# Optimization experiments

Measured on AMD Instinct MI355X. Metric: run time of the kernel, lower is better.

The kernel has to match this reference:

```python
import jax, jax.numpy as jnp
import numpy as np

B, N = 1, 320  # embed_dim == seq_len == N is forced by the module's bmm shapes


def setup_inputs() -> dict:
    key = jax.random.key(0)
    k1, k2, k3, k4 = jax.random.split(key, 4)
    s = jax.random.normal(k1, (B, N, N), dtype=jnp.float32)
    futrue = jax.random.normal(k2, (B, N, N, N), dtype=jnp.float32)
    # nn.Linear(embed_dim, embed_dim) params
    lim = 1.0 / np.sqrt(N)
    W = jax.random.uniform(k3, (N, N), minval=-lim, maxval=lim, dtype=jnp.float32)
    b = jax.random.uniform(k4, (N,), minval=-lim, maxval=lim, dtype=jnp.float32)
    return {"s": s, "futrue": futrue, "W": W, "b": b}


def reference(s, futrue, W, b):
    # futrue = self.fc(futrue): Linear on last dim  [B,T,T,E]
    futP = jnp.einsum('bitj,ej->bite', futrue, W) + b
    # fc = s.transpose(1,2) @ futrue : [B,1,E,T] @ [B,T,T,E] -> [B,T,E,E]
    scores = jnp.einsum('bte,bitj->biej', s, futP)
    fc = jax.nn.softmax(scores, axis=-1)          # softmax over last dim
    # vectorized loop: t_i = fc[:, i].sum(1).unsqueeze(-2).bmm(s)
    w = fc.sum(axis=2)                            # [B, T, T] (sum over e)
    out = jnp.einsum('bij,bjk->bik', w, s)        # concat of all t_i -> [B, T, E]
    return out
```

## Files before the change

kernel.cpp:

```cpp
#include <hip/hip_runtime.h>
#include <hip/hip_bf16.h>
#include <math.h>

#define N 320
#define NN (N * N)
#define SST 324
#define ZCNT (NN + N)

typedef float f32x16 __attribute__((ext_vector_type(16)));
typedef short s16x8  __attribute__((ext_vector_type(8)));

#define MFMA32(a, b, c) __builtin_amdgcn_mfma_f32_32x32x16_bf16((a), (b), (c), 0, 0, 0)

union U4V { uint4 q; s16x8 v; };
union UAV { unsigned u[4]; s16x8 v; };

__device__ inline void split2(float x0, float x1, unsigned& hi, unsigned& lo) {
    unsigned u0 = __float_as_uint(x0), u1 = __float_as_uint(x1);
    hi = (u0 >> 16) | (u1 & 0xFFFF0000u);
    float d0 = x0 - __uint_as_float(u0 & 0xFFFF0000u);
    float d1 = x1 - __uint_as_float(u1 & 0xFFFF0000u);
    lo = (__float_as_uint(d0) >> 16) | (__float_as_uint(d1) & 0xFFFF0000u);
}

__global__ __launch_bounds__(256) void zero_w_kernel(float* __restrict__ w) {
    int idx = blockIdx.x * 256 + threadIdx.x;
    if (idx * 4 < ZCNT) ((float4*)w)[idx] = make_float4(0.f, 0.f, 0.f, 0.f);
}

__global__ __launch_bounds__(64) void colsum_kernel(const float* __restrict__ s,
                                                    float* __restrict__ colsum) {
    int e = blockIdx.x * 64 + threadIdx.x;
    int t0 = blockIdx.y * 40;
    float a[8];
#pragma unroll
    for (int u = 0; u < 8; ++u) a[u] = 0.f;
    for (int t = 0; t < 40; t += 8) {
#pragma unroll
        for (int u = 0; u < 8; ++u) a[u] += s[(size_t)(t0 + t + u) * N + e];
    }
    float sum = ((a[0] + a[1]) + (a[2] + a[3])) + ((a[4] + a[5]) + (a[6] + a[7]));
    atomicAdd(&colsum[e], sum);
}

__global__ __launch_bounds__(64) void pack_s_kernel(const float* __restrict__ s,
                                                    uint4* __restrict__ spH,
                                                    uint4* __restrict__ spL) {
    int blk = blockIdx.x;
    int l = threadIdx.x;
    int et = blk / 20, ts = blk % 20;
    int e = et * 32 + (l & 31);
    int t0 = ts * 16 + (l >> 5) * 8;
    unsigned hi[4], lo[4];
#pragma unroll
    for (int d = 0; d < 4; ++d)
        split2(s[(size_t)(t0 + 2 * d) * N + e], s[(size_t)(t0 + 2 * d + 1) * N + e],
               hi[d], lo[d]);
    spH[blk * 64 + l] = make_uint4(hi[0], hi[1], hi[2], hi[3]);
    spL[blk * 64 + l] = make_uint4(lo[0], lo[1], lo[2], lo[3]);
}

__global__ __launch_bounds__(64) void pack_w_kernel(const float* __restrict__ W,
                                                    uint4* __restrict__ wpH,
                                                    uint4* __restrict__ wpL) {
    int blk = blockIdx.x;
    int l = threadIdx.x;
    int jt = blk / 20, ks = blk % 20;
    int j = jt * 32 + (l & 31);
    int k0 = ks * 16 + (l >> 5) * 8;
    const float* wr = W + (size_t)j * N + k0;
    unsigned hi[4], lo[4];
#pragma unroll
    for (int d = 0; d < 4; ++d) split2(wr[2 * d], wr[2 * d + 1], hi[d], lo[d]);
    wpH[blk * 64 + l] = make_uint4(hi[0], hi[1], hi[2], hi[3]);
    wpL[blk * 64 + l] = make_uint4(lo[0], lo[1], lo[2], lo[3]);
}

__global__ __launch_bounds__(640, 5) void fused_kernel(
    const float* __restrict__ fut,
    const uint4* __restrict__ spH, const uint4* __restrict__ spL,
    const uint4* __restrict__ wpH, const uint4* __restrict__ wpL,
    const float* __restrict__ bvec, const float* __restrict__ colsum,
    float* __restrict__ w)
{
    const int bid = blockIdx.x;
    const int i   = (bid / 80) * 8 + (bid & 7);
    const int et  = (bid >> 3) % 10;
    const int tid = threadIdx.x;
    const int wid = tid >> 6;
    const int lane = tid & 63;
    const int l31 = lane & 31;
    const int hf  = lane >> 5;

    __shared__ union {
        unsigned short G[2][40 * 32 * 8];
        float S[32 * SST];
    } sm;
    __shared__ float csh[32];
    __shared__ float Mfin[32];
    __shared__ float Ifin[32];

    if (tid < 32) csh[tid] = colsum[et * 32 + tid];

    f32x16 acc;
#pragma unroll
    for (int r = 0; r < 16; ++r) acc[r] = 0.f;

    const float* fbase = fut + (size_t)i * NN + (size_t)(hf * 8) * N + wid * 32 + l31;
    const uint4* aH = spH + (size_t)(et * 20) * 64 + lane;
    const uint4* aL = spL + (size_t)(et * 20) * 64 + lane;

    for (int ts = 0; ts < 20; ++ts) {
        const float* fp = fbase + (size_t)(ts * 16) * N;
        float f[8];
#pragma unroll
        for (int j = 0; j < 8; ++j) f[j] = fp[j * N];
        U4V ah; ah.q = aH[ts * 64];
        U4V al; al.q = aL[ts * 64];
        UAV bh, bl;
#pragma unroll
        for (int d = 0; d < 4; ++d) split2(f[2 * d], f[2 * d + 1], bh.u[d], bl.u[d]);
        acc = MFMA32(ah.v, bh.v, acc);
        acc = MFMA32(al.v, bh.v, acc);
        acc = MFMA32(ah.v, bl.v, acc);
    }

    {
        const int c  = wid * 4 + (l31 >> 3);
        const int jj = l31 & 7;
        const int sw = c & 7;
        unsigned short* GH = sm.G[0];
        unsigned short* GL = sm.G[1];
#pragma unroll
        for (int r = 0; r < 16; ++r) {
            int e = (r & 3) + ((r >> 2) << 3) + (hf << 2);
            float x = acc[r];
            unsigned u = __float_as_uint(x);
            float d = x - __uint_as_float(u & 0xFFFF0000u);
            int off = (c * 32 + (e ^ sw)) * 8 + jj;
            GH[off] = (unsigned short)(u >> 16);
            GL[off] = (unsigned short)(__float_as_uint(d) >> 16);
        }
    }
    __syncthreads();

    f32x16 acc2;
#pragma unroll
    for (int r = 0; r < 16; ++r) acc2[r] = 0.f;

    const uint4* bH = wpH + (size_t)(wid * 20) * 64 + lane;
    const uint4* bL = wpL + (size_t)(wid * 20) * 64 + lane;
    const unsigned short* GH = sm.G[0];
    const unsigned short* GL = sm.G[1];

#pragma unroll 4
    for (int ks = 0; ks < 20; ++ks) {
        int c0 = ks * 2 + hf;
        int aoff = (c0 * 32 + (l31 ^ (c0 & 7))) * 8;
        s16x8 gah = *(const s16x8*)&GH[aoff];
        s16x8 gal = *(const s16x8*)&GL[aoff];
        U4V wh; wh.q = bH[ks * 64];
        U4V wl; wl.q = bL[ks * 64];
        acc2 = MFMA32(gah, wh.v, acc2);
        acc2 = MFMA32(gal, wh.v, acc2);
        acc2 = MFMA32(gah, wl.v, acc2);
    }

    const int jcol = wid * 32 + l31;
    float bj = bvec[jcol];
    float v[16];
#pragma unroll
    for (int r = 0; r < 16; ++r) {
        int e = (r & 3) + ((r >> 2) << 3) + (hf << 2);
        v[r] = acc2[r] + csh[e] * bj;
    }

    __syncthreads();

#pragma unroll
    for (int r = 0; r < 16; ++r) {
        int e = (r & 3) + ((r >> 2) << 3) + (hf << 2);
        sm.S[e * SST + jcol] = v[r];
    }
    __syncthreads();

    const int hw = tid >> 5;
    const int li = tid & 31;
    if (hw < 16) {
#pragma unroll
        for (int rr = 0; rr < 2; ++rr) {
            int row = 2 * hw + rr;
            float x[10];
            float m = -3.4e38f;
#pragma unroll
            for (int q = 0; q < 10; ++q) {
                x[q] = sm.S[row * SST + li + 32 * q];
                m = fmaxf(m, x[q]);
            }
#pragma unroll
            for (int off = 16; off; off >>= 1) m = fmaxf(m, __shfl_xor(m, off, 64));
            float ssum = 0.f;
#pragma unroll
            for (int q = 0; q < 10; ++q) ssum += __expf(x[q] - m);
#pragma unroll
            for (int off = 16; off; off >>= 1) ssum += __shfl_xor(ssum, off, 64);
            if (li == 0) { Mfin[row] = m; Ifin[row] = 1.0f / ssum; }
        }
    }
    __syncthreads();

    float wcol = 0.f;
#pragma unroll
    for (int r = 0; r < 16; ++r) {
        int e = (r & 3) + ((r >> 2) << 3) + (hf << 2);
        wcol += __expf(v[r] - Mfin[e]) * Ifin[e];
    }
    wcol += __shfl_xor(wcol, 32, 64);
    if (hf == 0) atomicAdd(&w[(size_t)i * N + jcol], wcol);
}

__global__ __launch_bounds__(320) void out_gemm_kernel(
    const float* __restrict__ w, const float* __restrict__ s,
    float* __restrict__ out)
{
    const int i = blockIdx.x;
    const int k = threadIdx.x;
    const float* wr = w + (size_t)i * N;
    float a0 = 0.f, a1 = 0.f, a2 = 0.f, a3 = 0.f;
    for (int j = 0; j < N; j += 4) {
        a0 += wr[j + 0] * s[(size_t)(j + 0) * N + k];
        a1 += wr[j + 1] * s[(size_t)(j + 1) * N + k];
        a2 += wr[j + 2] * s[(size_t)(j + 2) * N + k];
        a3 += wr[j + 3] * s[(size_t)(j + 3) * N + k];
    }
    out[(size_t)i * N + k] = (a0 + a1) + (a2 + a3);
}

extern "C" void kernel_launch(void* const* d_in, const int* in_sizes, int n_in,
                              void* d_out, int out_size, void* d_ws, size_t ws_size,
                              hipStream_t stream)
{
    const float* s    = (const float*)d_in[0];
    const float* fut  = (const float*)d_in[1];
    const float* W    = (const float*)d_in[2];
    const float* bvec = (const float*)d_in[3];
    float* out = (float*)d_out;

    char* base = (char*)d_ws;
    float* wbuf   = (float*)base;
    float* colsum = (float*)(base + 409600);
    uint4* spH = (uint4*)(base + 410880);
    uint4* spL = (uint4*)(base + 615680);
    uint4* wpH = (uint4*)(base + 820480);
    uint4* wpL = (uint4*)(base + 1025280);

    zero_w_kernel<<<dim3((ZCNT / 4 + 255) / 256), dim3(256), 0, stream>>>(wbuf);
    colsum_kernel<<<dim3(5, 8), dim3(64), 0, stream>>>(s, colsum);
    pack_s_kernel<<<dim3(200), dim3(64), 0, stream>>>(s, spH, spL);
    pack_w_kernel<<<dim3(200), dim3(64), 0, stream>>>(W, wpH, wpL);

    fused_kernel<<<dim3(3200), dim3(640), 0, stream>>>(
        fut, spH, spL, wpH, wpL, bvec, colsum, wbuf);

    out_gemm_kernel<<<dim3(N), dim3(320), 0, stream>>>(wbuf, s, out);
}
```

Measured before the change: 386.7 us.

## Process two e-tiles per block to halve futrue reads and fuse prep kernels

The main kernel now computes two 32-wide e slabs per block from one pass over the futrue tile, so each futrue element is loaded and split into bf16 hi/lo half as often and the grid shrinks from 3200 to 1600 blocks. The four small setup kernels are merged into one prep kernel, which also zeroes the output buffer, cutting launch overhead. The output GEMM is split four ways over j and accumulates with atomics for more parallelism. In exchange, the main kernel holds two MFMA accumulators, which raises register pressure, and it runs the softmax stage twice with extra block barriers.

Result: slower. 414.7 us (+7.2%).

```diff
diff --git a/kernel.cpp b/kernel.cpp
--- a/kernel.cpp
+++ b/kernel.cpp
@@ -5,7 +5,6 @@
 #define N 320
 #define NN (N * N)
 #define SST 324
-#define ZCNT (NN + N)
 
 typedef float f32x16 __attribute__((ext_vector_type(16)));
 typedef short s16x8  __attribute__((ext_vector_type(8)));
@@ -23,60 +22,60 @@
     lo = (__float_as_uint(d0) >> 16) | (__float_as_uint(d1) & 0xFFFF0000u);
 }
 
-__global__ __launch_bounds__(256) void zero_w_kernel(float* __restrict__ w) {
-    int idx = blockIdx.x * 256 + threadIdx.x;
-    if (idx * 4 < ZCNT) ((float4*)w)[idx] = make_float4(0.f, 0.f, 0.f, 0.f);
-}
-
-__global__ __launch_bounds__(64) void colsum_kernel(const float* __restrict__ s,
-                                                    float* __restrict__ colsum) {
-    int e = blockIdx.x * 64 + threadIdx.x;
-    int t0 = blockIdx.y * 40;
-    float a[8];
-#pragma unroll
-    for (int u = 0; u < 8; ++u) a[u] = 0.f;
-    for (int t = 0; t < 40; t += 8) {
-#pragma unroll
-        for (int u = 0; u < 8; ++u) a[u] += s[(size_t)(t0 + t + u) * N + e];
+__global__ __launch_bounds__(256) void prep_kernel(
+    const float* __restrict__ s, const float* __restrict__ W,
+    float* __restrict__ wbuf, float* __restrict__ out, float* __restrict__ colsum,
+    uint4* __restrict__ spH, uint4* __restrict__ spL,
+    uint4* __restrict__ wpH, uint4* __restrict__ wpL)
+{
+    const int bid = blockIdx.x;
+    const int tid = threadIdx.x;
+    if (bid < 100) {
+        ((float4*)wbuf)[bid * 256 + tid] = make_float4(0.f, 0.f, 0.f, 0.f);
+    } else if (bid < 200) {
+        ((float4*)out)[(bid - 100) * 256 + tid] = make_float4(0.f, 0.f, 0.f, 0.f);
+    } else if (bid < 202) {
+        int e = (bid - 200) * 256 + tid;
+        if (e < N) {
+            const float* sp = s + e;
+            float a[8];
+#pragma unroll
+            for (int u = 0; u < 8; ++u) a[u] = 0.f;
+            for (int t = 0; t < N; t += 8) {
+#pragma unroll
+                for (int u = 0; u < 8; ++u) a[u] += sp[(size_t)(t + u) * N];
+            }
+            colsum[e] = ((a[0] + a[1]) + (a[2] + a[3])) + ((a[4] + a[5]) + (a[6] + a[7]));
+        }
+    } else if (bid < 252) {
+        int sub = (bid - 202) * 4 + (tid >> 6);
+        int l = tid & 63;
+        int et = sub / 20, ts = sub % 20;
+        int e = et * 32 + (l & 31);
+        int t0 = ts * 16 + (l >> 5) * 8;
+        unsigned hi[4], lo[4];
+#pragma unroll
+        for (int d = 0; d < 4; ++d)
+            split2(s[(size_t)(t0 + 2 * d) * N + e], s[(size_t)(t0 + 2 * d + 1) * N + e],
+                   hi[d], lo[d]);
+        spH[sub * 64 + l] = make_uint4(hi[0], hi[1], hi[2], hi[3]);
+        spL[sub * 64 + l] = make_uint4(lo[0], lo[1], lo[2], lo[3]);
+    } else {
+        int sub = (bid - 252) * 4 + (tid >> 6);
+        int l = tid & 63;
+        int jt = sub / 20, ks = sub % 20;
+        int j = jt * 32 + (l & 31);
+        int k0 = ks * 16 + (l >> 5) * 8;
+        const float* wr = W + (size_t)j * N + k0;
+        unsigned hi[4], lo[4];
+#pragma unroll
+        for (int d = 0; d < 4; ++d) split2(wr[2 * d], wr[2 * d + 1], hi[d], lo[d]);
+        wpH[sub * 64 + l] = make_uint4(hi[0], hi[1], hi[2], hi[3]);
+        wpL[sub * 64 + l] = make_uint4(lo[0], lo[1], lo[2], lo[3]);
     }
-    float sum = ((a[0] + a[1]) + (a[2] + a[3])) + ((a[4] + a[5]) + (a[6] + a[7]));
-    atomicAdd(&colsum[e], sum);
-}
-
-__global__ __launch_bounds__(64) void pack_s_kernel(const float* __restrict__ s,
-                                                    uint4* __restrict__ spH,
-                                                    uint4* __restrict__ spL) {
-    int blk = blockIdx.x;
-    int l = threadIdx.x;
-    int et = blk / 20, ts = blk % 20;
-    int e = et * 32 + (l & 31);
-    int t0 = ts * 16 + (l >> 5) * 8;
-    unsigned hi[4], lo[4];
-#pragma unroll
-    for (int d = 0; d < 4; ++d)
-        split2(s[(size_t)(t0 + 2 * d) * N + e], s[(size_t)(t0 + 2 * d + 1) * N + e],
-               hi[d], lo[d]);
-    spH[blk * 64 + l] = make_uint4(hi[0], hi[1], hi[2], hi[3]);
-    spL[blk * 64 + l] = make_uint4(lo[0], lo[1], lo[2], lo[3]);
-}
-
-__global__ __launch_bounds__(64) void pack_w_kernel(const float* __restrict__ W,
-                                                    uint4* __restrict__ wpH,
-                                                    uint4* __restrict__ wpL) {
-    int blk = blockIdx.x;
-    int l = threadIdx.x;
-    int jt = blk / 20, ks = blk % 20;
-    int j = jt * 32 + (l & 31);
-    int k0 = ks * 16 + (l >> 5) * 8;
-    const float* wr = W + (size_t)j * N + k0;
-    unsigned hi[4], lo[4];
-#pragma unroll
-    for (int d = 0; d < 4; ++d) split2(wr[2 * d], wr[2 * d + 1], hi[d], lo[d]);
-    wpH[blk * 64 + l] = make_uint4(hi[0], hi[1], hi[2], hi[3]);
-    wpL[blk * 64 + l] = make_uint4(lo[0], lo[1], lo[2], lo[3]);
-}
-
-__global__ __launch_bounds__(640, 5) void fused_kernel(
+}
+
+__global__ __launch_bounds__(640, 5) void fused5_kernel(
     const float* __restrict__ fut,
     const uint4* __restrict__ spH, const uint4* __restrict__ spL,
     const uint4* __restrict__ wpH, const uint4* __restrict__ wpL,
@@ -84,8 +83,10 @@
     float* __restrict__ w)
 {
     const int bid = blockIdx.x;
-    const int i   = (bid / 80) * 8 + (bid & 7);
-    const int et  = (bid >> 3) % 10;
+    const int x  = bid & 7;
+    const int g  = bid >> 3;
+    const int iw = g / 5, eq = g % 5;
+    const int i  = iw * 8 + x;
     const int tid = threadIdx.x;
     const int wid = tid >> 6;
     const int lane = tid & 63;
@@ -96,125 +97,137 @@
         unsigned short G[2][40 * 32 * 8];
         float S[32 * SST];
     } sm;
-    __shared__ float csh[32];
+    __shared__ float csh[64];
     __shared__ float Mfin[32];
     __shared__ float Ifin[32];
 
-    if (tid < 32) csh[tid] = colsum[et * 32 + tid];
-
-    f32x16 acc;
-#pragma unroll
-    for (int r = 0; r < 16; ++r) acc[r] = 0.f;
+    if (tid < 64) csh[tid] = colsum[eq * 64 + tid];
+
+    f32x16 acc0, acc1;
+#pragma unroll
+    for (int r = 0; r < 16; ++r) { acc0[r] = 0.f; acc1[r] = 0.f; }
 
     const float* fbase = fut + (size_t)i * NN + (size_t)(hf * 8) * N + wid * 32 + l31;
-    const uint4* aH = spH + (size_t)(et * 20) * 64 + lane;
-    const uint4* aL = spL + (size_t)(et * 20) * 64 + lane;
-
+    const uint4* aH0 = spH + (size_t)((eq * 2 + 0) * 20) * 64 + lane;
+    const uint4* aL0 = spL + (size_t)((eq * 2 + 0) * 20) * 64 + lane;
+    const uint4* aH1 = spH + (size_t)((eq * 2 + 1) * 20) * 64 + lane;
+    const uint4* aL1 = spL + (size_t)((eq * 2 + 1) * 20) * 64 + lane;
+
+#pragma unroll 2
     for (int ts = 0; ts < 20; ++ts) {
         const float* fp = fbase + (size_t)(ts * 16) * N;
         float f[8];
 #pragma unroll
-        for (int j = 0; j < 8; ++j) f[j] = fp[j * N];
-        U4V ah; ah.q = aH[ts * 64];
-        U4V al; al.q = aL[ts * 64];
+        for (int m = 0; m < 8; ++m) f[m] = fp[(size_t)m * N];
         UAV bh, bl;
 #pragma unroll
         for (int d = 0; d < 4; ++d) split2(f[2 * d], f[2 * d + 1], bh.u[d], bl.u[d]);
-        acc = MFMA32(ah.v, bh.v, acc);
-        acc = MFMA32(al.v, bh.v, acc);
-        acc = MFMA32(ah.v, bl.v, acc);
+        U4V a0h, a0l, a1h, a1l;
+        a0h.q = aH0[ts * 64]; a0l.q = aL0[ts * 64];
+        a1h.q = aH1[ts * 64]; a1l.q = aL1[ts * 64];
+        acc0 = MFMA32(a0h.v, bh.v, acc0);
+        acc1 = MFMA32(a1h.v, bh.v, acc1);
+        acc0 = MFMA32(a0l.v, bh.v, acc0);
+        acc1 = MFMA32(a1l.v, bh.v, acc1);
+        acc0 = MFMA32(a0h.v, bl.v, acc0);
+        acc1 = MFMA32(a1h.v, bl.v, acc1);
     }
 
-    {
-        const int c  = wid * 4 + (l31 >> 3);
-        const int jj = l31 & 7;
-        const int sw = c & 7;
-        unsigned short* GH = sm.G[0];
-        unsigned short* GL = sm.G[1];
+    const uint4* bHp = wpH + (size_t)(wid * 20) * 64 + lane;
+    const uint4* bLp = wpL + (size_t)(wid * 20) * 64 + lane;
+    const int jcol = wid * 32 + l31;
+    const float bj = bvec[jcol];
+    const int hw = tid >> 5;
+    const int li = tid & 31;
+    float wcol = 0.f;
+
+    auto doSlab = [&](const f32x16& acc, const int slab) {
+        {
+            const int c  = wid * 4 + (l31 >> 3);
+            const int jj = l31 & 7;
+            const int sw = c & 7;
+            unsigned short* GH = sm.G[0];
+            unsigned short* GL = sm.G[1];
+#pragma unroll
+            for (int r = 0; r < 16; ++r) {
+                int e = (r & 3) + ((r >> 2) << 3) + (hf << 2);
+                float xv = acc[r];
+                unsigned u = __float_as_uint(xv);
+                float d = xv - __uint_as_float(u & 0xFFFF0000u);
+                int off = (c * 32 + (e ^ sw)) * 8 + jj;
+                GH[off] = (unsigned short)(u >> 16);
+                GL[off] = (unsigned short)(__float_as_uint(d) >> 16);
+            }
+        }
+        __syncthreads();
+
+        f32x16 p;
+#pragma unroll
+        for (int r = 0; r < 16; ++r) p[r] = 0.f;
+        const unsigned short* GH = sm.G[0];
+        const unsigned short* GL = sm.G[1];
+#pragma unroll 4
+        for (int ks = 0; ks < 20; ++ks) {
+            int c = ks * 2 + hf;
+            int off = (c * 32 + (l31 ^ (c & 7))) * 8;
+            s16x8 gh = *(const s16x8*)&GH[off];
+            s16x8 gl = *(const s16x8*)&GL[off];
+            U4V wh, wl;
+            wh.q = bHp[ks * 64];
+            wl.q = bLp[ks * 64];
+            p = MFMA32(gh, wh.v, p);
+            p = MFMA32(gl, wh.v, p);
+            p = MFMA32(gh, wl.v, p);
+        }
+
+        float v[16];
 #pragma unroll
         for (int r = 0; r < 16; ++r) {
             int e = (r & 3) + ((r >> 2) << 3) + (hf << 2);
-            float x = acc[r];
-            unsigned u = __float_as_uint(x);
-            float d = x - __uint_as_float(u & 0xFFFF0000u);
-            int off = (c * 32 + (e ^ sw)) * 8 + jj;
-            GH[off] = (unsigned short)(u >> 16);
-            GL[off] = (unsigned short)(__float_as_uint(d) >> 16);
-        }
-    }
-    __syncthreads();
-
-    f32x16 acc2;
-#pragma unroll
-    for (int r = 0; r < 16; ++r) acc2[r] = 0.f;
-
-    const uint4* bH = wpH + (size_t)(wid * 20) * 64 + lane;
-    const uint4* bL = wpL + (size_t)(wid * 20) * 64 + lane;
-    const unsigned short* GH = sm.G[0];
-    const unsigned short* GL = sm.G[1];
-
-#pragma unroll 4
-    for (int ks = 0; ks < 20; ++ks) {
-        int c0 = ks * 2 + hf;
-        int aoff = (c0 * 32 + (l31 ^ (c0 & 7))) * 8;
-        s16x8 gah = *(const s16x8*)&GH[aoff];
-        s16x8 gal = *(const s16x8*)&GL[aoff];
-        U4V wh; wh.q = bH[ks * 64];
-        U4V wl; wl.q = bL[ks * 64];
-        acc2 = MFMA32(gah, wh.v, acc2);
-        acc2 = MFMA32(gal, wh.v, acc2);
-        acc2 = MFMA32(gah, wl.v, acc2);
-    }
-
-    const int jcol = wid * 32 + l31;
-    float bj = bvec[jcol];
-    float v[16];
-#pragma unroll
-    for (int r = 0; r < 16; ++r) {
-        int e = (r & 3) + ((r >> 2) << 3) + (hf << 2);
-        v[r] = acc2[r] + csh[e] * bj;
-    }
-
-    __syncthreads();
-
-#pragma unroll
-    for (int r = 0; r < 16; ++r) {
-        int e = (r & 3) + ((r >> 2) << 3) + (hf << 2);
-        sm.S[e * SST + jcol] = v[r];
-    }
-    __syncthreads();
-
-    const int hw = tid >> 5;
-    const int li = tid & 31;
-    if (hw < 16) {
-#pragma unroll
-        for (int rr = 0; rr < 2; ++rr) {
-            int row = 2 * hw + rr;
-            float x[10];
-            float m = -3.4e38f;
-#pragma unroll
-            for (int q = 0; q < 10; ++q) {
-                x[q] = sm.S[row * SST + li + 32 * q];
-                m = fmaxf(m, x[q]);
+            v[r] = p[r] + csh[slab * 32 + e] * bj;
+        }
+        __syncthreads();
+
+#pragma unroll
+        for (int r = 0; r < 16; ++r) {
+            int e = (r & 3) + ((r >> 2) << 3) + (hf << 2);
+            sm.S[e * SST + jcol] = v[r];
+        }
+        __syncthreads();
+
+        if (hw < 16) {
+#pragma unroll
+            for (int rr = 0; rr < 2; ++rr) {
+                int row = 2 * hw + rr;
+                float xr[10];
+                float m = -3.4e38f;
+#pragma unroll
+                for (int q = 0; q < 10; ++q) {
+                    xr[q] = sm.S[row * SST + li + 32 * q];
+                    m = fmaxf(m, xr[q]);
+                }
+#pragma unroll
+                for (int off = 16; off; off >>= 1) m = fmaxf(m, __shfl_xor(m, off, 64));
+                float ssum = 0.f;
+#pragma unroll
+                for (int q = 0; q < 10; ++q) ssum += __expf(xr[q] - m);
+#pragma unroll
+                for (int off = 16; off; off >>= 1) ssum += __shfl_xor(ssum, off, 64);
+                if (li == 0) { Mfin[row] = m; Ifin[row] = 1.0f / ssum; }
             }
-#pragma unroll
-            for (int off = 16; off; off >>= 1) m = fmaxf(m, __shfl_xor(m, off, 64));
-            float ssum = 0.f;
-#pragma unroll
-            for (int q = 0; q < 10; ++q) ssum += __expf(x[q] - m);
-#pragma unroll
-            for (int off = 16; off; off >>= 1) ssum += __shfl_xor(ssum, off, 64);
-            if (li == 0) { Mfin[row] = m; Ifin[row] = 1.0f / ssum; }
-        }
-    }
-    __syncthreads();
-
-    float wcol = 0.f;
-#pragma unroll
-    for (int r = 0; r < 16; ++r) {
-        int e = (r & 3) + ((r >> 2) << 3) + (hf << 2);
-        wcol += __expf(v[r] - Mfin[e]) * Ifin[e];
-    }
+        }
+        __syncthreads();
+
+#pragma unroll
+        for (int r = 0; r < 16; ++r) {
+            int e = (r & 3) + ((r >> 2) << 3) + (hf << 2);
+            wcol += __expf(v[r] - Mfin[e]) * Ifin[e];
+        }
+    };
+
+    doSlab(acc0, 0);
+    doSlab(acc1, 1);
+
     wcol += __shfl_xor(wcol, 32, 64);
     if (hf == 0) atomicAdd(&w[(size_t)i * N + jcol], wcol);
 }
@@ -224,16 +237,18 @@
     float* __restrict__ out)
 {
     const int i = blockIdx.x;
+    const int jc = blockIdx.y;
     const int k = threadIdx.x;
-    const float* wr = w + (size_t)i * N;
+    const float* wr = w + (size_t)i * N + jc * 80;
+    const float* sp = s + (size_t)(jc * 80) * N + k;
     float a0 = 0.f, a1 = 0.f, a2 = 0.f, a3 = 0.f;
-    for (int j = 0; j < N; j += 4) {
-        a0 += wr[j + 0] * s[(size_t)(j + 0) * N + k];
-        a1 += wr[j + 1] * s[(size_t)(j + 1) * N + k];
-        a2 += wr[j + 2] * s[(size_t)(j + 2) * N + k];
-        a3 += wr[j + 3] * s[(size_t)(j + 3) * N + k];
+    for (int j = 0; j < 80; j += 4) {
+        a0 += wr[j + 0] * sp[(size_t)(j + 0) * N];
+        a1 += wr[j + 1] * sp[(size_t)(j + 1) * N];
+        a2 += wr[j + 2] * sp[(size_t)(j + 2) * N];
+        a3 += wr[j + 3] * sp[(size_t)(j + 3) * N];
     }
-    out[(size_t)i * N + k] = (a0 + a1) + (a2 + a3);
+    atomicAdd(&out[(size_t)i * N + k], (a0 + a1) + (a2 + a3));
 }
 
 extern "C" void kernel_launch(void* const* d_in, const int* in_sizes, int n_in,
@@ -254,13 +269,11 @@
     uint4* wpH = (uint4*)(base + 820480);
     uint4* wpL = (uint4*)(base + 1025280);
 
-    zero_w_kernel<<<dim3((ZCNT / 4 + 255) / 256), dim3(256), 0, stream>>>(wbuf);
-    colsum_kernel<<<dim3(5, 8), dim3(64), 0, stream>>>(s, colsum);
-    pack_s_kernel<<<dim3(200), dim3(64), 0, stream>>>(s, spH, spL);
-    pack_w_kernel<<<dim3(200), dim3(64), 0, stream>>>(W, wpH, wpL);
-
-    fused_kernel<<<dim3(3200), dim3(640), 0, stream>>>(
+    prep_kernel<<<dim3(302), dim3(256), 0, stream>>>(
+        s, W, wbuf, out, colsum, spH, spL, wpH, wpL);
+
+    fused5_kernel<<<dim3(1600), dim3(640), 0, stream>>>(
         fut, spH, spL, wpH, wpL, bvec, colsum, wbuf);
 
-    out_gemm_kernel<<<dim3(N), dim3(320), 0, stream>>>(wbuf, s, out);
-}
+    out_gemm_kernel<<<dim3(N, 4), dim3(320), 0, stream>>>(wbuf, s, out);
+}
```
